# Performance work log

Measured on AMD Instinct MI355X. Metric: run time of the kernel, lower is better.

Reference implementation:

```python
import jax, jax.numpy as jnp
import numpy as np

N_NODES = 50000
N_EDGES = 800000
IN_C = 16
HID_C = 16
OUT_C = 10
N_GRAPHS = 500
EDGE_DIM = 3
MLP_HID = 25
BN_EPS = 1e-5


def setup_inputs() -> dict:
    key = jax.random.key(0)
    ks = iter(jax.random.split(key, 40))

    def nrm(shape, scale=1.0):
        return jax.random.normal(next(ks), shape, dtype=jnp.float32) * scale

    inp = {}
    inp["x"] = nrm((N_NODES, IN_C))
    inp["edge_index"] = jax.random.randint(next(ks), (2, N_EDGES), 0, N_NODES, dtype=jnp.int32)
    inp["edge_attr"] = jax.random.uniform(next(ks), (N_EDGES, EDGE_DIM), dtype=jnp.float32)
    inp["batch"] = jnp.sort(jax.random.randint(next(ks), (N_NODES,), 0, N_GRAPHS, dtype=jnp.int32))

    def bn_params():
        g = jax.random.uniform(next(ks), (MLP_HID,), minval=0.8, maxval=1.2, dtype=jnp.float32)
        b = nrm((MLP_HID,), 0.1)
        mu = nrm((MLP_HID,), 0.1)
        var = jax.random.uniform(next(ks), (MLP_HID,), minval=0.5, maxval=1.5, dtype=jnp.float32)
        return g, b, mu, var

    # edge MLP 1: 3 -> 25 -> IN_C*HID_C
    inp["W1a"] = nrm((EDGE_DIM, MLP_HID), 0.3)
    inp["b1a"] = nrm((MLP_HID,), 0.05)
    inp["g1"], inp["bt1"], inp["m1"], inp["v1"] = bn_params()
    inp["W1b"] = nrm((MLP_HID, IN_C * HID_C), 0.1)
    inp["b1b"] = nrm((IN_C * HID_C,), 0.05)
    inp["root1"] = nrm((IN_C, HID_C), 0.2)
    inp["bias1"] = nrm((HID_C,), 0.05)

    # edge MLP 2: 3 -> 25 -> HID_C*HID_C
    inp["W2a"] = nrm((EDGE_DIM, MLP_HID), 0.3)
    inp["b2a"] = nrm((MLP_HID,), 0.05)
    inp["g2"], inp["bt2"], inp["m2"], inp["v2"] = bn_params()
    inp["W2b"] = nrm((MLP_HID, HID_C * HID_C), 0.1)
    inp["b2b"] = nrm((HID_C * HID_C,), 0.05)
    inp["root2"] = nrm((HID_C, HID_C), 0.2)
    inp["bias2"] = nrm((HID_C,), 0.05)

    # final MLP([HID_C, OUT_C]) -> single plain linear (plain_last)
    inp["fcW"] = nrm((HID_C, OUT_C), 0.2)
    inp["fcb"] = nrm((OUT_C,), 0.05)
    return inp


def _edge_mlp(e, Wa, ba, g, bt, mu, var, Wb, bb):
    # Linear -> BatchNorm(eval) -> ReLU -> (dropout=eval identity) -> Linear
    h = e @ Wa + ba
    h = g * (h - mu) * jax.lax.rsqrt(var + BN_EPS) + bt
    h = jax.nn.relu(h)
    return h @ Wb + bb


def _nnconv(x, src, dst, w_edge, root, bias, out_dim):
    # message: x_j [E,in] times per-edge weight [E,in,out]
    msg = jnp.einsum("ei,eio->eo", x[src], w_edge)
    agg = jax.ops.segment_sum(msg, dst, num_segments=N_NODES)
    deg = jax.ops.segment_sum(jnp.ones((src.shape[0],), msg.dtype), dst, num_segments=N_NODES)
    agg = agg / jnp.maximum(deg, 1.0)[:, None]  # mean aggregation
    return agg + x @ root + bias


def reference(x, edge_index, edge_attr, batch,
              W1a, b1a, g1, bt1, m1, v1, W1b, b1b, root1, bias1,
              W2a, b2a, g2, bt2, m2, v2, W2b, b2b, root2, bias2,
              fcW, fcb):
    src, dst = edge_index[0], edge_index[1]

    w1 = _edge_mlp(edge_attr, W1a, b1a, g1, bt1, m1, v1, W1b, b1b).reshape(-1, IN_C, HID_C)
    x = jax.nn.elu(_nnconv(x, src, dst, w1, root1, bias1, HID_C))

    w2 = _edge_mlp(edge_attr, W2a, b2a, g2, bt2, m2, v2, W2b, b2b).reshape(-1, HID_C, HID_C)
    x = jax.nn.elu(_nnconv(x, src, dst, w2, root2, bias2, HID_C))

    # global mean pooling over graphs
    pooled = jax.ops.segment_sum(x, batch, num_segments=N_GRAPHS)
    cnt = jax.ops.segment_sum(jnp.ones((x.shape[0],), x.dtype), batch, num_segments=N_GRAPHS)
    pooled = pooled / jnp.maximum(cnt, 1.0)[:, None]

    return pooled @ fcW + fcb  # [N_GRAPHS, OUT_C]
```

## Files before the change

### kernel.cpp

```cpp
#include <hip/hip_runtime.h>
#include <math.h>

#define N_NODES 50000
#define N_EDGES 800000
#define IN_C 16
#define HID_C 16
#define OUT_C 10
#define N_GRAPHS 500
#define EDGE_DIM 3
#define MLP_HID 25
#define BN_EPS 1e-5f

#define SCAN_NB ((N_NODES + 255) / 256)
#define NZB 200

typedef __attribute__((ext_vector_type(8))) _Float16 half8;
typedef __attribute__((ext_vector_type(2))) _Float16 half2v;
typedef __attribute__((ext_vector_type(4))) float f32x4;
union U4H8 { uint4 u; half8 h; half2v p[4]; };
union HU { _Float16 h; unsigned short u; };


__global__ __launch_bounds__(256) void setup_kernel(
    const float* __restrict__ W1a, const float* __restrict__ b1a,
    const float* __restrict__ g1, const float* __restrict__ bt1,
    const float* __restrict__ m1, const float* __restrict__ v1,
    const float* __restrict__ W2a, const float* __restrict__ b2a,
    const float* __restrict__ g2, const float* __restrict__ bt2,
    const float* __restrict__ m2, const float* __restrict__ v2,
    const float* __restrict__ W1b, const float* __restrict__ b1b,
    const float* __restrict__ W2b, const float* __restrict__ b2b,
    const int* __restrict__ batch,
    const float* __restrict__ xin, const float* __restrict__ eattr,
    float* __restrict__ AC1, float* __restrict__ AC2,
    unsigned int* __restrict__ WF1, unsigned int* __restrict__ WF2,
    int* __restrict__ goff, int* __restrict__ cnt,
    float4* __restrict__ ea4, unsigned int* __restrict__ xh0,
    int* __restrict__ ticket)
{
    const int blk = blockIdx.x;
    const int tid = threadIdx.x;
    if (blk < 7) {
        int t = blk * 256 + tid;
        if (t >= 1664) return;
        const float *Wb, *bb; unsigned int *WH;
        int tl = t;
        if (t < 832) { Wb = W1b; bb = b1b; WH = WF1; }
        else { tl = t - 832; Wb = W2b; bb = b2b; WH = WF2; }
        int m = tl >> 6;
        int L = tl & 63;
        int q = L >> 4, o = L & 15;
        unsigned int hi[8];
        for (int j = 0; j < 8; ++j) {
            int kp = m*32 + q*8 + j;
            int k = kp >> 4, i = kp & 15;
            float w = (k < 25) ? Wb[k*256 + i*16 + o] : bb[i*16 + o];
            HU cv; cv.h = (_Float16)w;
            hi[j] = cv.u;
        }
        int base = (m*64 + L) * 4;
        for (int d = 0; d < 4; ++d)
            WH[base + d] = hi[2*d] | (hi[2*d+1] << 16);
        return;
    }
    if (blk == 7 || blk == 8) {
        if (blk == 7) {
            if (tid < 26) {
                int k = tid;
                if (k < 25) {
                    float sc = g1[k] / sqrtf(v1[k] + BN_EPS);
                    AC1[k*4+0] = sc * W1a[0*MLP_HID+k];
                    AC1[k*4+1] = sc * W1a[1*MLP_HID+k];
                    AC1[k*4+2] = sc * W1a[2*MLP_HID+k];
                    AC1[k*4+3] = sc * (b1a[k] - m1[k]) + bt1[k];
                } else {
                    AC1[100] = 0.f; AC1[101] = 0.f; AC1[102] = 0.f; AC1[103] = 1.f;
                }
            } else if (tid >= 32 && tid < 58) {
                int k = tid - 32;
                if (k < 25) {
                    float sc = g2[k] / sqrtf(v2[k] + BN_EPS);
                    AC2[k*4+0] = sc * W2a[0*MLP_HID+k];
                    AC2[k*4+1] = sc * W2a[1*MLP_HID+k];
                    AC2[k*4+2] = sc * W2a[2*MLP_HID+k];
                    AC2[k*4+3] = sc * (b2a[k] - m2[k]) + bt2[k];
                } else {
                    AC2[100] = 0.f; AC2[101] = 0.f; AC2[102] = 0.f; AC2[103] = 1.f;
                }
            }
        }
        int g = (blk - 7) * 256 + tid;
        if (g <= N_GRAPHS) {
            int lo = 0, hi = N_NODES;
            while (lo < hi) {
                int mid = (lo + hi) >> 1;
                if (batch[mid] < g) lo = mid + 1; else hi = mid;
            }
            goff[g] = lo;
        }
        return;
    }
    const int bt = (blk - 9) * 256 + tid;
    const int STR = NZB * 256;
    int4* c4 = (int4*)cnt;
    const int4 z4 = {0, 0, 0, 0};
    for (int i = bt; i < 12500; i += STR) c4[i] = z4;
    for (int e = bt; e < N_EDGES; e += STR) {
        float4 a;
        a.x = eattr[e*3+0];
        a.y = eattr[e*3+1];
        a.z = eattr[e*3+2];
        a.w = 0.f;
        ea4[e] = a;
    }
    const float2* x2 = (const float2*)xin;
    for (int i = bt; i < 400000; i += STR) {
        float2 v = x2[i];
        HU h0; h0.h = (_Float16)v.x;
        HU h1; h1.h = (_Float16)v.y;
        xh0[i] = (unsigned int)h0.u | ((unsigned int)h1.u << 16);
    }
    if (blk == 9 && tid == 0) *ticket = 0;
}


__global__ __launch_bounds__(256) void rank_kernel(const int* __restrict__ dst,
                                                   int* __restrict__ cnt,
                                                   int* __restrict__ rank) {
    int e = blockIdx.x * blockDim.x + threadIdx.x;
    if (e < N_EDGES) rank[e] = atomicAdd(&cnt[dst[e]], 1);
}

__global__ __launch_bounds__(256) void scan_p1(const int* __restrict__ cnt,
                                               int* __restrict__ bsum,
                                               int* __restrict__ bpre,
                                               int* __restrict__ off,
                                               int* __restrict__ ticket) {
    __shared__ int lds[256];
    __shared__ int sDone;
    int t = threadIdx.x;
    int idx = blockIdx.x * 256 + t;
    lds[t] = (idx < N_NODES) ? cnt[idx] : 0;
    __syncthreads();
    for (int d = 128; d > 0; d >>= 1) {
        if (t < d) lds[t] += lds[t + d];
        __syncthreads();
    }
    if (t == 0) {
        bsum[blockIdx.x] = lds[0];
        __threadfence();
        sDone = atomicAdd(ticket, 1);
    }
    __syncthreads();
    if (sDone != SCAN_NB - 1) return;
    __threadfence();
    int v = (t < SCAN_NB) ? bsum[t] : 0;
    __syncthreads();
    lds[t] = v;
    __syncthreads();
    for (int d = 1; d < 256; d <<= 1) {
        int u = (t >= d) ? lds[t - d] : 0;
        __syncthreads();
        lds[t] += u;
        __syncthreads();
    }
    if (t < SCAN_NB) bpre[t] = (t > 0) ? lds[t - 1] : 0;
    if (t == 255) off[N_NODES] = lds[255];
}

__global__ __launch_bounds__(256) void scan_p3(const int* __restrict__ cnt,
                                               const int* __restrict__ bpre,
                                               int* __restrict__ off) {
    __shared__ int lds[256];
    int t = threadIdx.x;
    int idx = blockIdx.x * 256 + t;
    int v = (idx < N_NODES) ? cnt[idx] : 0;
    lds[t] = v;
    __syncthreads();
    for (int d = 1; d < 256; d <<= 1) {
        int u = (t >= d) ? lds[t - d] : 0;
        __syncthreads();
        lds[t] += u;
        __syncthreads();
    }
    if (idx < N_NODES) off[idx] = bpre[blockIdx.x] + lds[t] - v;
}


__global__ __launch_bounds__(256) void edge_mfma7_kernel(
    const unsigned short* __restrict__ xh,
    const int* __restrict__ src,
    const int* __restrict__ dst,
    const int* __restrict__ rank,
    const int* __restrict__ off,
    const float4* __restrict__ ea4,
    const float* __restrict__ AC,
    const unsigned int* __restrict__ WF,
    float* __restrict__ msg_buf)
{
    __shared__ uint4 wf_s[832];
    const int tid = threadIdx.x;
    #pragma unroll
    for (int it = 0; it < 4; ++it) {
        int gi = tid + it*256;
        if (gi < 832) wf_s[gi] = ((const uint4*)WF)[gi];
    }
    __syncthreads();

    const int wave = tid >> 6;
    const int lane = tid & 63;
    const int q    = lane >> 4;
    const int el   = lane & 15;
    const int i0   = (q & 1) * 8;
    const bool bsel = (q >> 1) != 0;
    const int E0   = (blockIdx.x * 4 + wave) * 64;

    const int sAll = src[E0 + lane];
    const int dAll = dst[E0 + lane];
    const int rAll = rank[E0 + lane];
    const int pAll = off[dAll] + rAll;

    int   sT[4];
    float a0[4], a1[4], a2[4];
    #pragma unroll
    for (int t = 0; t < 4; ++t) {
        sT[t] = __shfl(sAll, t*16 + el);
        float4 at = ea4[E0 + t*16 + el];
        a0[t] = at.x; a1[t] = at.y; a2[t] = at.z;
    }

    U4H8 xf[4];
    #pragma unroll
    for (int t = 0; t < 4; ++t)
        xf[t].u = *(const uint4*)(const void*)(xh + (size_t)sT[t]*16 + i0);

    f32x4 acc0 = {0.f,0.f,0.f,0.f}, acc1 = {0.f,0.f,0.f,0.f};
    f32x4 acc2 = {0.f,0.f,0.f,0.f}, acc3 = {0.f,0.f,0.f,0.f};
    #pragma unroll 1
    for (int m = 0; m < 13; ++m) {
        const float4 Ae = *(const float4*)(AC + m*8);
        const float4 Ao = *(const float4*)(AC + m*8 + 4);
        const float A0 = bsel ? Ao.x : Ae.x;
        const float A1 = bsel ? Ao.y : Ae.y;
        const float A2 = bsel ? Ao.z : Ae.z;
        const float A3 = bsel ? Ao.w : Ae.w;
        U4H8 w; w.u = wf_s[m*64 + lane];
        #pragma unroll
        for (int t = 0; t < 4; ++t) {
            float h = fmaxf(fmaf(a2[t], A2, fmaf(a1[t], A1,
                              fmaf(a0[t], A0, A3))), 0.f);
            _Float16 hh = (_Float16)h;
            half2v h2; h2.x = hh; h2.y = hh;
            U4H8 f;
            #pragma unroll
            for (int j = 0; j < 4; ++j) f.p[j] = h2 * xf[t].p[j];
            f32x4 a = (t==0) ? acc0 : (t==1) ? acc1 : (t==2) ? acc2 : acc3;
            a = __builtin_amdgcn_mfma_f32_16x16x32_f16(w.h, f.h, a, 0, 0, 0);
            if (t==0) acc0 = a; else if (t==1) acc1 = a;
            else if (t==2) acc2 = a; else acc3 = a;
        }
    }

    #pragma unroll
    for (int t = 0; t < 4; ++t) {
        int row = __shfl(pAll, t*16 + el);
        f32x4 a = (t==0) ? acc0 : (t==1) ? acc1 : (t==2) ? acc2 : acc3;
        *(f32x4*)(msg_buf + (size_t)row * HID_C + q*4) = a;
    }
}

__global__ __launch_bounds__(256) void node_gather_kernel(
    const float* __restrict__ xin, const float* __restrict__ msg_buf,
    const int* __restrict__ off,
    const float* __restrict__ root, const float* __restrict__ bias,
    float* __restrict__ xout, unsigned int* __restrict__ xh_out)
{
    __shared__ float root_s[IN_C * HID_C];
    if (threadIdx.x < 64)
        ((float4*)root_s)[threadIdx.x] = ((const float4*)root)[threadIdx.x];
    __syncthreads();

    int t = blockIdx.x * blockDim.x + threadIdx.x;
    int n = t >> 2;
    if (n >= N_NODES) return;
    int c0 = (t & 3) * 4;
    int lo = off[n], hi = off[n+1];
    float inv = 1.f / fmaxf((float)(hi - lo), 1.f);

    const f32x4* m4 = (const f32x4*)msg_buf;
    const int qi = c0 >> 2;
    f32x4 s0 = {0.f,0.f,0.f,0.f}, s1 = {0.f,0.f,0.f,0.f};
    int r = lo;
    for (; r + 2 <= hi; r += 2) {
        s0 += m4[(size_t)r*4 + qi];
        s1 += m4[(size_t)(r+1)*4 + qi];
    }
    if (r < hi) s0 += m4[(size_t)r*4 + qi];
    f32x4 s = s0 + s1;

    const float4 bv = *(const float4*)(bias + c0);
    f32x4 acc;
    acc.x = fmaf(s.x, inv, bv.x);
    acc.y = fmaf(s.y, inv, bv.y);
    acc.z = fmaf(s.z, inv, bv.z);
    acc.w = fmaf(s.w, inv, bv.w);

    const float4* x4 = (const float4*)(xin + (size_t)n * IN_C);
    #pragma unroll
    for (int j = 0; j < 4; ++j) {
        float4 xv = x4[j];
        #pragma unroll
        for (int k = 0; k < 4; ++k) {
            float xi = (k==0) ? xv.x : (k==1) ? xv.y : (k==2) ? xv.z : xv.w;
            const float4 rv = *(const float4*)(root_s + (j*4+k)*HID_C + c0);
            acc.x = fmaf(xi, rv.x, acc.x);
            acc.y = fmaf(xi, rv.y, acc.y);
            acc.z = fmaf(xi, rv.z, acc.z);
            acc.w = fmaf(xi, rv.w, acc.w);
        }
    }

    acc.x = acc.x > 0.f ? acc.x : (expf(acc.x) - 1.f);
    acc.y = acc.y > 0.f ? acc.y : (expf(acc.y) - 1.f);
    acc.z = acc.z > 0.f ? acc.z : (expf(acc.z) - 1.f);
    acc.w = acc.w > 0.f ? acc.w : (expf(acc.w) - 1.f);
    *(f32x4*)(xout + (size_t)n * HID_C + c0) = acc;

    if (xh_out) {
        HU h0, h1, h2, h3;
        h0.h = (_Float16)acc.x; h1.h = (_Float16)acc.y;
        h2.h = (_Float16)acc.z; h3.h = (_Float16)acc.w;
        uint2 pk;
        pk.x = (unsigned int)h0.u | ((unsigned int)h1.u << 16);
        pk.y = (unsigned int)h2.u | ((unsigned int)h3.u << 16);
        ((uint2*)xh_out)[n*4 + qi] = pk;
    }
}

__global__ __launch_bounds__(64) void pool_final_kernel(
    const float* __restrict__ xin, const int* __restrict__ goff,
    const float* __restrict__ fcW, const float* __restrict__ fcb,
    float* __restrict__ out)
{
    __shared__ float part[4][HID_C];
    __shared__ float pooled[HID_C];
    int g = blockIdx.x;
    int t = threadIdx.x;
    int c = t & 15, sub = t >> 4;
    int lo = goff[g], hi = goff[g+1];
    float s = 0.f;
    for (int n = lo + sub; n < hi; n += 4)
        s += xin[(size_t)n*HID_C + c];
    part[sub][c] = s;
    __syncthreads();
    if (t < HID_C) {
        pooled[t] = (part[0][t] + part[1][t] + part[2][t] + part[3][t])
                    / fmaxf((float)(hi - lo), 1.f);
    }
    __syncthreads();
    if (t < OUT_C) {
        float acc = fcb[t];
        #pragma unroll
        for (int i = 0; i < HID_C; ++i)
            acc = fmaf(pooled[i], fcW[i*OUT_C+t], acc);
        out[g*OUT_C + t] = acc;
    }
}


extern "C" void kernel_launch(void* const* d_in, const int* in_sizes, int n_in,
                              void* d_out, int out_size, void* d_ws, size_t ws_size,
                              hipStream_t stream)
{
    const float* x     = (const float*)d_in[0];
    const int*   ei    = (const int*)d_in[1];
    const float* eattr = (const float*)d_in[2];
    const int*   batch = (const int*)d_in[3];
    const float* W1a   = (const float*)d_in[4];
    const float* b1a   = (const float*)d_in[5];
    const float* g1    = (const float*)d_in[6];
    const float* bt1   = (const float*)d_in[7];
    const float* m1    = (const float*)d_in[8];
    const float* v1    = (const float*)d_in[9];
    const float* W1b   = (const float*)d_in[10];
    const float* b1b   = (const float*)d_in[11];
    const float* root1 = (const float*)d_in[12];
    const float* bias1 = (const float*)d_in[13];
    const float* W2a   = (const float*)d_in[14];
    const float* b2a   = (const float*)d_in[15];
    const float* g2    = (const float*)d_in[16];
    const float* bt2   = (const float*)d_in[17];
    const float* m2    = (const float*)d_in[18];
    const float* v2    = (const float*)d_in[19];
    const float* W2b   = (const float*)d_in[20];
    const float* b2b   = (const float*)d_in[21];
    const float* root2 = (const float*)d_in[22];
    const float* bias2 = (const float*)d_in[23];
    const float* fcW   = (const float*)d_in[24];
    const float* fcb   = (const float*)d_in[25];

    const int* src = ei;
    const int* dst = ei + N_EDGES;

    float* ws   = (float*)d_ws;
    float* MSG  = ws;
    float* X1   = ws + 12800000;
    float* X2   = ws + 13600000;
    int*   RANK = (int*)(ws + 14400000);
    int*   CNT  = (int*)(ws + 15200000);
    int*   OFF  = (int*)(ws + 15250000);
    int*   GOFF = (int*)(ws + 15300064);
    unsigned int* WF1 = (unsigned int*)(ws + 15300576);
    unsigned int* WF2 = (unsigned int*)(ws + 15303904);
    float* AC1  = ws + 15307232;
    float* AC2  = ws + 15307344;
    int*   BSUM = (int*)(ws + 15307456);
    int*   BPRE = (int*)(ws + 15307712);
    int*   TICK = (int*)(ws + 15307968);
    float* EA4  = ws + 15308032;
    unsigned int* XH0 = (unsigned int*)(ws + 18508032);
    unsigned int* XH1 = (unsigned int*)(ws + 18908032);

    setup_kernel<<<9 + NZB, 256, 0, stream>>>(
        W1a, b1a, g1, bt1, m1, v1, W2a, b2a, g2, bt2, m2, v2,
        W1b, b1b, W2b, b2b, batch, x, eattr,
        AC1, AC2, WF1, WF2, GOFF, CNT, (float4*)EA4, XH0, TICK);
    rank_kernel<<<N_EDGES/256, 256, 0, stream>>>(dst, CNT, RANK);
    scan_p1<<<SCAN_NB, 256, 0, stream>>>(CNT, BSUM, BPRE, OFF, TICK);
    scan_p3<<<SCAN_NB, 256, 0, stream>>>(CNT, BPRE, OFF);

    edge_mfma7_kernel<<<N_EDGES/256, 256, 0, stream>>>(
        (const unsigned short*)XH0, src, dst, RANK, OFF,
        (const float4*)EA4, AC1, WF1, MSG);
    node_gather_kernel<<<(N_NODES*4 + 255)/256, 256, 0, stream>>>(
        x, MSG, OFF, root1, bias1, X1, XH1);

    edge_mfma7_kernel<<<N_EDGES/256, 256, 0, stream>>>(
        (const unsigned short*)XH1, src, dst, RANK, OFF,
        (const float4*)EA4, AC2, WF2, MSG);
    node_gather_kernel<<<(N_NODES*4 + 255)/256, 256, 0, stream>>>(
        X1, MSG, OFF, root2, bias2, X2, (unsigned int*)nullptr);

    pool_final_kernel<<<N_GRAPHS, 64, 0, stream>>>(X2, GOFF, fcW, fcb, (float*)d_out);
}
```

Measured before the change: 251.4 us.

## Pre-permute edges into CSR order once and store messages in fp16

Adds a permute kernel that scatters src indices and padded edge attributes into destination-sorted order once. Both edge MFMA passes then read contiguously and write messages at their own position instead of scattering through off/rank lookups. Messages are stored as fp16 rather than fp32, halving message write and read traffic in the node gather. The cost is an extra kernel with a scattered write, plus reduced precision in the per-edge messages before mean aggregation.

```diff
diff --git a/kernel.cpp b/kernel.cpp
--- a/kernel.cpp
+++ b/kernel.cpp
@@ -19,6 +19,15 @@
 typedef __attribute__((ext_vector_type(4))) float f32x4;
 union U4H8 { uint4 u; half8 h; half2v p[4]; };
 union HU { _Float16 h; unsigned short u; };
+union UH2 { unsigned int u; half2v h; };
+
+static __device__ inline f32x4 unpack_h4(uint2 v) {
+    UH2 a, b; a.u = v.x; b.u = v.y;
+    f32x4 r;
+    r.x = (float)a.h.x; r.y = (float)a.h.y;
+    r.z = (float)b.h.x; r.w = (float)b.h.y;
+    return r;
+}
 
 
 __global__ __launch_bounds__(256) void setup_kernel(
@@ -30,13 +39,11 @@
     const float* __restrict__ m2, const float* __restrict__ v2,
     const float* __restrict__ W1b, const float* __restrict__ b1b,
     const float* __restrict__ W2b, const float* __restrict__ b2b,
-    const int* __restrict__ batch,
-    const float* __restrict__ xin, const float* __restrict__ eattr,
+    const int* __restrict__ batch, const float* __restrict__ xin,
     float* __restrict__ AC1, float* __restrict__ AC2,
     unsigned int* __restrict__ WF1, unsigned int* __restrict__ WF2,
     int* __restrict__ goff, int* __restrict__ cnt,
-    float4* __restrict__ ea4, unsigned int* __restrict__ xh0,
-    int* __restrict__ ticket)
+    unsigned int* __restrict__ xh0, int* __restrict__ ticket)
 {
     const int blk = blockIdx.x;
     const int tid = threadIdx.x;
@@ -105,14 +112,6 @@
     int4* c4 = (int4*)cnt;
     const int4 z4 = {0, 0, 0, 0};
     for (int i = bt; i < 12500; i += STR) c4[i] = z4;
-    for (int e = bt; e < N_EDGES; e += STR) {
-        float4 a;
-        a.x = eattr[e*3+0];
-        a.y = eattr[e*3+1];
-        a.z = eattr[e*3+2];
-        a.w = 0.f;
-        ea4[e] = a;
-    }
     const float2* x2 = (const float2*)xin;
     for (int i = bt; i < 400000; i += STR) {
         float2 v = x2[i];
@@ -186,17 +185,32 @@
     if (idx < N_NODES) off[idx] = bpre[blockIdx.x] + lds[t] - v;
 }
 
-
-__global__ __launch_bounds__(256) void edge_mfma7_kernel(
+__global__ __launch_bounds__(256) void permute_kernel(
+    const int* __restrict__ src, const int* __restrict__ dst,
+    const int* __restrict__ rank, const int* __restrict__ off,
+    const float* __restrict__ eattr,
+    int* __restrict__ ssrc, float4* __restrict__ ea4p)
+{
+    int e = blockIdx.x * blockDim.x + threadIdx.x;
+    int d = dst[e];
+    int p = off[d] + rank[e];
+    ssrc[p] = src[e];
+    float4 a;
+    a.x = eattr[e*3+0];
+    a.y = eattr[e*3+1];
+    a.z = eattr[e*3+2];
+    a.w = 0.f;
+    ea4p[p] = a;
+}
+
+
+__global__ __launch_bounds__(256) void edge_mfma8_kernel(
     const unsigned short* __restrict__ xh,
-    const int* __restrict__ src,
-    const int* __restrict__ dst,
-    const int* __restrict__ rank,
-    const int* __restrict__ off,
-    const float4* __restrict__ ea4,
+    const int* __restrict__ ssrc,
+    const float4* __restrict__ ea4p,
     const float* __restrict__ AC,
     const unsigned int* __restrict__ WF,
-    float* __restrict__ msg_buf)
+    unsigned int* __restrict__ msg16)
 {
     __shared__ uint4 wf_s[832];
     const int tid = threadIdx.x;
@@ -213,19 +227,16 @@
     const int el   = lane & 15;
     const int i0   = (q & 1) * 8;
     const bool bsel = (q >> 1) != 0;
-    const int E0   = (blockIdx.x * 4 + wave) * 64;
-
-    const int sAll = src[E0 + lane];
-    const int dAll = dst[E0 + lane];
-    const int rAll = rank[E0 + lane];
-    const int pAll = off[dAll] + rAll;
+    const int P0   = (blockIdx.x * 4 + wave) * 64;
+
+    const int sAll = ssrc[P0 + lane];
 
     int   sT[4];
     float a0[4], a1[4], a2[4];
     #pragma unroll
     for (int t = 0; t < 4; ++t) {
         sT[t] = __shfl(sAll, t*16 + el);
-        float4 at = ea4[E0 + t*16 + el];
+        float4 at = ea4p[P0 + t*16 + el];
         a0[t] = at.x; a1[t] = at.y; a2[t] = at.z;
     }
 
@@ -263,14 +274,19 @@
 
     #pragma unroll
     for (int t = 0; t < 4; ++t) {
-        int row = __shfl(pAll, t*16 + el);
         f32x4 a = (t==0) ? acc0 : (t==1) ? acc1 : (t==2) ? acc2 : acc3;
-        *(f32x4*)(msg_buf + (size_t)row * HID_C + q*4) = a;
+        HU c0, c1, c2, c3;
+        c0.h = (_Float16)a.x; c1.h = (_Float16)a.y;
+        c2.h = (_Float16)a.z; c3.h = (_Float16)a.w;
+        uint2 pk;
+        pk.x = (unsigned int)c0.u | ((unsigned int)c1.u << 16);
+        pk.y = (unsigned int)c2.u | ((unsigned int)c3.u << 16);
+        ((uint2*)msg16)[(size_t)(P0 + t*16 + el) * 4 + q] = pk;
     }
 }
 
 __global__ __launch_bounds__(256) void node_gather_kernel(
-    const float* __restrict__ xin, const float* __restrict__ msg_buf,
+    const float* __restrict__ xin, const unsigned int* __restrict__ msg16,
     const int* __restrict__ off,
     const float* __restrict__ root, const float* __restrict__ bias,
     float* __restrict__ xout, unsigned int* __restrict__ xh_out)
@@ -287,15 +303,15 @@
     int lo = off[n], hi = off[n+1];
     float inv = 1.f / fmaxf((float)(hi - lo), 1.f);
 
-    const f32x4* m4 = (const f32x4*)msg_buf;
+    const uint2* m2 = (const uint2*)msg16;
     const int qi = c0 >> 2;
     f32x4 s0 = {0.f,0.f,0.f,0.f}, s1 = {0.f,0.f,0.f,0.f};
     int r = lo;
     for (; r + 2 <= hi; r += 2) {
-        s0 += m4[(size_t)r*4 + qi];
-        s1 += m4[(size_t)(r+1)*4 + qi];
-    }
-    if (r < hi) s0 += m4[(size_t)r*4 + qi];
+        s0 += unpack_h4(m2[(size_t)r*4 + qi]);
+        s1 += unpack_h4(m2[(size_t)(r+1)*4 + qi]);
+    }
+    if (r < hi) s0 += unpack_h4(m2[(size_t)r*4 + qi]);
     f32x4 s = s0 + s1;
 
     const float4 bv = *(const float4*)(bias + c0);
@@ -403,43 +419,44 @@
     const int* dst = ei + N_EDGES;
 
     float* ws   = (float*)d_ws;
-    float* MSG  = ws;
-    float* X1   = ws + 12800000;
-    float* X2   = ws + 13600000;
-    int*   RANK = (int*)(ws + 14400000);
-    int*   CNT  = (int*)(ws + 15200000);
-    int*   OFF  = (int*)(ws + 15250000);
-    int*   GOFF = (int*)(ws + 15300064);
-    unsigned int* WF1 = (unsigned int*)(ws + 15300576);
-    unsigned int* WF2 = (unsigned int*)(ws + 15303904);
-    float* AC1  = ws + 15307232;
-    float* AC2  = ws + 15307344;
-    int*   BSUM = (int*)(ws + 15307456);
-    int*   BPRE = (int*)(ws + 15307712);
-    int*   TICK = (int*)(ws + 15307968);
-    float* EA4  = ws + 15308032;
-    unsigned int* XH0 = (unsigned int*)(ws + 18508032);
-    unsigned int* XH1 = (unsigned int*)(ws + 18908032);
+    unsigned int* MSG16 = (unsigned int*)ws;
+    float* X1   = ws + 6400000;
+    float* X2   = ws + 7200000;
+    int*   RANK = (int*)(ws + 8000000);
+    int*   CNT  = (int*)(ws + 8800000);
+    int*   OFF  = (int*)(ws + 8850000);
+    int*   GOFF = (int*)(ws + 8900064);
+    unsigned int* WF1 = (unsigned int*)(ws + 8900576);
+    unsigned int* WF2 = (unsigned int*)(ws + 8903904);
+    float* AC1  = ws + 8907232;
+    float* AC2  = ws + 8907344;
+    int*   BSUM = (int*)(ws + 8907456);
+    int*   BPRE = (int*)(ws + 8907712);
+    int*   TICK = (int*)(ws + 8907968);
+    int*   SSRC = (int*)(ws + 8908032);
+    float* EA4P = ws + 9708032;
+    unsigned int* XH0 = (unsigned int*)(ws + 12908032);
+    unsigned int* XH1 = (unsigned int*)(ws + 13308032);
 
     setup_kernel<<<9 + NZB, 256, 0, stream>>>(
         W1a, b1a, g1, bt1, m1, v1, W2a, b2a, g2, bt2, m2, v2,
-        W1b, b1b, W2b, b2b, batch, x, eattr,
-        AC1, AC2, WF1, WF2, GOFF, CNT, (float4*)EA4, XH0, TICK);
+        W1b, b1b, W2b, b2b, batch, x,
+        AC1, AC2, WF1, WF2, GOFF, CNT, XH0, TICK);
     rank_kernel<<<N_EDGES/256, 256, 0, stream>>>(dst, CNT, RANK);
     scan_p1<<<SCAN_NB, 256, 0, stream>>>(CNT, BSUM, BPRE, OFF, TICK);
     scan_p3<<<SCAN_NB, 256, 0, stream>>>(CNT, BPRE, OFF);
-
-    edge_mfma7_kernel<<<N_EDGES/256, 256, 0, stream>>>(
-        (const unsigned short*)XH0, src, dst, RANK, OFF,
-        (const float4*)EA4, AC1, WF1, MSG);
+    permute_kernel<<<N_EDGES/256, 256, 0, stream>>>(src, dst, RANK, OFF, eattr,
+                                                    SSRC, (float4*)EA4P);
+
+    edge_mfma8_kernel<<<N_EDGES/256, 256, 0, stream>>>(
+        (const unsigned short*)XH0, SSRC, (const float4*)EA4P, AC1, WF1, MSG16);
     node_gather_kernel<<<(N_NODES*4 + 255)/256, 256, 0, stream>>>(
-        x, MSG, OFF, root1, bias1, X1, XH1);
-
-    edge_mfma7_kernel<<<N_EDGES/256, 256, 0, stream>>>(
-        (const unsigned short*)XH1, src, dst, RANK, OFF,
-        (const float4*)EA4, AC2, WF2, MSG);
+        x, MSG16, OFF, root1, bias1, X1, XH1);
+
+    edge_mfma8_kernel<<<N_EDGES/256, 256, 0, stream>>>(
+        (const unsigned short*)XH1, SSRC, (const float4*)EA4P, AC2, WF2, MSG16);
     node_gather_kernel<<<(N_NODES*4 + 255)/256, 256, 0, stream>>>(
-        X1, MSG, OFF, root2, bias2, X2, (unsigned int*)nullptr);
+        X1, MSG16, OFF, root2, bias2, X2, (unsigned int*)nullptr);
 
     pool_final_kernel<<<N_GRAPHS, 64, 0, stream>>>(X2, GOFF, fcW, fcb, (float*)d_out);
 }
```

Result: slower. 263.6 us (+4.8%).

## Fuse all stages into one persistent kernel with grid-wide barriers

Applied to the files above, without the earlier changes.

Replaces the nine separate kernel launches (setup, rank, two scan passes, two edge/node pairs, pooling) with one persistent kernel of 256 blocks of 1024 threads. Stages are separated by a software grid barrier built on atomic counters. The scan is rewritten as wave-level shuffle scans over int4 chunks, and pooling runs one graph per wave. This removes launch gaps and tail effects between kernels. In exchange it adds spin-wait barrier cost, assumes all 256 blocks are co-resident, and gives the edge and node phases fewer threads per block with grid-stride loops.

```diff
diff --git a/kernel.cpp b/kernel.cpp
--- a/kernel.cpp
+++ b/kernel.cpp
@@ -11,8 +11,11 @@
 #define MLP_HID 25
 #define BN_EPS 1e-5f
 
-#define SCAN_NB ((N_NODES + 255) / 256)
-#define NZB 200
+#define GRID 256
+#define BLKT 1024
+#define GSZ (GRID * BLKT)
+#define NWAVES (GRID * (BLKT / 64))
+#define NCHUNK 196
 
 typedef __attribute__((ext_vector_type(8))) _Float16 half8;
 typedef __attribute__((ext_vector_type(2))) _Float16 half2v;
@@ -20,29 +23,203 @@
 union U4H8 { uint4 u; half8 h; half2v p[4]; };
 union HU { _Float16 h; unsigned short u; };
 
-
-__global__ __launch_bounds__(256) void setup_kernel(
+__device__ __forceinline__ void gbar(int* bar, int* gen) {
+    __syncthreads();
+    if (threadIdx.x == 0) {
+        __threadfence();
+        int g = __hip_atomic_load(gen, __ATOMIC_RELAXED, __HIP_MEMORY_SCOPE_AGENT);
+        int a = __hip_atomic_fetch_add(bar, 1, __ATOMIC_ACQ_REL, __HIP_MEMORY_SCOPE_AGENT);
+        if (a == GRID - 1) {
+            __hip_atomic_store(bar, 0, __ATOMIC_RELAXED, __HIP_MEMORY_SCOPE_AGENT);
+            __hip_atomic_fetch_add(gen, 1, __ATOMIC_RELEASE, __HIP_MEMORY_SCOPE_AGENT);
+        } else {
+            while (__hip_atomic_load(gen, __ATOMIC_ACQUIRE, __HIP_MEMORY_SCOPE_AGENT) == g) {
+                __builtin_amdgcn_s_sleep(1);
+            }
+        }
+        __threadfence();
+    }
+    __syncthreads();
+}
+
+__device__ __forceinline__ void edge_phase(
+    const unsigned short* __restrict__ xh,
+    const int* __restrict__ src, const int* __restrict__ dst,
+    const int* __restrict__ rank, const int* __restrict__ off,
+    const float4* __restrict__ ea4, const float* __restrict__ AC,
+    const unsigned int* __restrict__ WF, float* __restrict__ msg_buf,
+    uint4* wf_s, int tid)
+{
+    for (int gi = tid; gi < 832; gi += BLKT)
+        wf_s[gi] = ((const uint4*)WF)[gi];
+    __syncthreads();
+
+    const int wave = tid >> 6;
+    const int lane = tid & 63;
+    const int q    = lane >> 4;
+    const int el   = lane & 15;
+    const int i0   = (q & 1) * 8;
+    const bool bsel = (q >> 1) != 0;
+    const int gw   = blockIdx.x * (BLKT / 64) + wave;
+
+    for (int v = gw; v < N_EDGES / 64; v += NWAVES) {
+        const int E0 = v * 64;
+        const int sAll = src[E0 + lane];
+        const int dAll = dst[E0 + lane];
+        const int rAll = rank[E0 + lane];
+        const int pAll = off[dAll] + rAll;
+
+        int   sT[4];
+        float a0[4], a1[4], a2[4];
+        #pragma unroll
+        for (int t = 0; t < 4; ++t) {
+            sT[t] = __shfl(sAll, t*16 + el);
+            float4 at = ea4[E0 + t*16 + el];
+            a0[t] = at.x; a1[t] = at.y; a2[t] = at.z;
+        }
+
+        U4H8 xf[4];
+        #pragma unroll
+        for (int t = 0; t < 4; ++t)
+            xf[t].u = *(const uint4*)(const void*)(xh + (size_t)sT[t]*16 + i0);
+
+        f32x4 acc0 = {0.f,0.f,0.f,0.f}, acc1 = {0.f,0.f,0.f,0.f};
+        f32x4 acc2 = {0.f,0.f,0.f,0.f}, acc3 = {0.f,0.f,0.f,0.f};
+        #pragma unroll 1
+        for (int m = 0; m < 13; ++m) {
+            const float4 Ae = *(const float4*)(AC + m*8);
+            const float4 Ao = *(const float4*)(AC + m*8 + 4);
+            const float A0 = bsel ? Ao.x : Ae.x;
+            const float A1 = bsel ? Ao.y : Ae.y;
+            const float A2 = bsel ? Ao.z : Ae.z;
+            const float A3 = bsel ? Ao.w : Ae.w;
+            U4H8 w; w.u = wf_s[m*64 + lane];
+            #pragma unroll
+            for (int t = 0; t < 4; ++t) {
+                float h = fmaxf(fmaf(a2[t], A2, fmaf(a1[t], A1,
+                                  fmaf(a0[t], A0, A3))), 0.f);
+                _Float16 hh = (_Float16)h;
+                half2v h2; h2.x = hh; h2.y = hh;
+                U4H8 f;
+                #pragma unroll
+                for (int j = 0; j < 4; ++j) f.p[j] = h2 * xf[t].p[j];
+                f32x4 a = (t==0) ? acc0 : (t==1) ? acc1 : (t==2) ? acc2 : acc3;
+                a = __builtin_amdgcn_mfma_f32_16x16x32_f16(w.h, f.h, a, 0, 0, 0);
+                if (t==0) acc0 = a; else if (t==1) acc1 = a;
+                else if (t==2) acc2 = a; else acc3 = a;
+            }
+        }
+
+        #pragma unroll
+        for (int t = 0; t < 4; ++t) {
+            int row = __shfl(pAll, t*16 + el);
+            f32x4 a = (t==0) ? acc0 : (t==1) ? acc1 : (t==2) ? acc2 : acc3;
+            *(f32x4*)(msg_buf + (size_t)row * HID_C + q*4) = a;
+        }
+    }
+}
+
+__device__ __forceinline__ void node_phase(
+    const float* __restrict__ xin, const float* __restrict__ msg_buf,
+    const int* __restrict__ off, const float* root_s,
+    const float* __restrict__ bias,
+    float* __restrict__ xout, unsigned int* __restrict__ xh_out, int gt)
+{
+    for (int t = gt; t < N_NODES * 4; t += GSZ) {
+        int n = t >> 2;
+        int c0 = (t & 3) * 4;
+        int lo = off[n], hi = off[n+1];
+        float inv = 1.f / fmaxf((float)(hi - lo), 1.f);
+
+        const f32x4* m4 = (const f32x4*)msg_buf;
+        const int qi = t & 3;
+        f32x4 s0 = {0.f,0.f,0.f,0.f}, s1 = {0.f,0.f,0.f,0.f};
+        int r = lo;
+        for (; r + 2 <= hi; r += 2) {
+            s0 += m4[(size_t)r*4 + qi];
+            s1 += m4[(size_t)(r+1)*4 + qi];
+        }
+        if (r < hi) s0 += m4[(size_t)r*4 + qi];
+        f32x4 s = s0 + s1;
+
+        const float4 bv = *(const float4*)(bias + c0);
+        f32x4 acc;
+        acc.x = fmaf(s.x, inv, bv.x);
+        acc.y = fmaf(s.y, inv, bv.y);
+        acc.z = fmaf(s.z, inv, bv.z);
+        acc.w = fmaf(s.w, inv, bv.w);
+
+        const float4* x4 = (const float4*)(xin + (size_t)n * IN_C);
+        #pragma unroll
+        for (int j = 0; j < 4; ++j) {
+            float4 xv = x4[j];
+            #pragma unroll
+            for (int k = 0; k < 4; ++k) {
+                float xi = (k==0) ? xv.x : (k==1) ? xv.y : (k==2) ? xv.z : xv.w;
+                const float4 rv = *(const float4*)(root_s + (j*4+k)*HID_C + c0);
+                acc.x = fmaf(xi, rv.x, acc.x);
+                acc.y = fmaf(xi, rv.y, acc.y);
+                acc.z = fmaf(xi, rv.z, acc.z);
+                acc.w = fmaf(xi, rv.w, acc.w);
+            }
+        }
+
+        acc.x = acc.x > 0.f ? acc.x : (expf(acc.x) - 1.f);
+        acc.y = acc.y > 0.f ? acc.y : (expf(acc.y) - 1.f);
+        acc.z = acc.z > 0.f ? acc.z : (expf(acc.z) - 1.f);
+        acc.w = acc.w > 0.f ? acc.w : (expf(acc.w) - 1.f);
+        *(f32x4*)(xout + (size_t)n * HID_C + c0) = acc;
+
+        if (xh_out) {
+            HU h0, h1, h2, h3;
+            h0.h = (_Float16)acc.x; h1.h = (_Float16)acc.y;
+            h2.h = (_Float16)acc.z; h3.h = (_Float16)acc.w;
+            uint2 pk;
+            pk.x = (unsigned int)h0.u | ((unsigned int)h1.u << 16);
+            pk.y = (unsigned int)h2.u | ((unsigned int)h3.u << 16);
+            ((uint2*)xh_out)[n*4 + qi] = pk;
+        }
+    }
+}
+
+__global__ __launch_bounds__(BLKT) void mega_kernel(
+    const float* __restrict__ xin, const int* __restrict__ src,
+    const int* __restrict__ dst, const float* __restrict__ eattr,
+    const int* __restrict__ batch,
     const float* __restrict__ W1a, const float* __restrict__ b1a,
     const float* __restrict__ g1, const float* __restrict__ bt1,
     const float* __restrict__ m1, const float* __restrict__ v1,
+    const float* __restrict__ W1b, const float* __restrict__ b1b,
+    const float* __restrict__ root1, const float* __restrict__ bias1,
     const float* __restrict__ W2a, const float* __restrict__ b2a,
     const float* __restrict__ g2, const float* __restrict__ bt2,
     const float* __restrict__ m2, const float* __restrict__ v2,
-    const float* __restrict__ W1b, const float* __restrict__ b1b,
     const float* __restrict__ W2b, const float* __restrict__ b2b,
-    const int* __restrict__ batch,
-    const float* __restrict__ xin, const float* __restrict__ eattr,
-    float* __restrict__ AC1, float* __restrict__ AC2,
-    unsigned int* __restrict__ WF1, unsigned int* __restrict__ WF2,
-    int* __restrict__ goff, int* __restrict__ cnt,
-    float4* __restrict__ ea4, unsigned int* __restrict__ xh0,
-    int* __restrict__ ticket)
+    const float* __restrict__ root2, const float* __restrict__ bias2,
+    const float* __restrict__ fcW, const float* __restrict__ fcb,
+    float* __restrict__ MSG, float* __restrict__ X1, float* __restrict__ X2,
+    int* __restrict__ RANK, int* __restrict__ CNT, int* __restrict__ OFF,
+    int* __restrict__ GOFF, unsigned int* __restrict__ WF1,
+    unsigned int* __restrict__ WF2, float* __restrict__ AC1,
+    float* __restrict__ AC2, int* __restrict__ BSUM, int* __restrict__ BPRE,
+    float4* __restrict__ EA4, unsigned int* __restrict__ XH0,
+    unsigned int* __restrict__ XH1, float* __restrict__ out,
+    int* __restrict__ ctrl)
 {
-    const int blk = blockIdx.x;
-    const int tid = threadIdx.x;
-    if (blk < 7) {
-        int t = blk * 256 + tid;
-        if (t >= 1664) return;
+    __shared__ uint4 wf_s[832];
+    __shared__ float root_s[IN_C * HID_C];
+    __shared__ int   sc[256];
+
+    const int tid  = threadIdx.x;
+    const int gt   = blockIdx.x * BLKT + tid;
+    const int wave = tid >> 6;
+    const int lane = tid & 63;
+    const int gw   = blockIdx.x * (BLKT / 64) + wave;
+    int* bar = ctrl;
+    int* gen = ctrl + 1;
+
+    if (gt < 1664) {
+        int t = gt;
         const float *Wb, *bb; unsigned int *WH;
         int tl = t;
         if (t < 832) { Wb = W1b; bb = b1b; WH = WF1; }
@@ -61,309 +238,154 @@
         int base = (m*64 + L) * 4;
         for (int d = 0; d < 4; ++d)
             WH[base + d] = hi[2*d] | (hi[2*d+1] << 16);
-        return;
-    }
-    if (blk == 7 || blk == 8) {
-        if (blk == 7) {
-            if (tid < 26) {
-                int k = tid;
-                if (k < 25) {
-                    float sc = g1[k] / sqrtf(v1[k] + BN_EPS);
-                    AC1[k*4+0] = sc * W1a[0*MLP_HID+k];
-                    AC1[k*4+1] = sc * W1a[1*MLP_HID+k];
-                    AC1[k*4+2] = sc * W1a[2*MLP_HID+k];
-                    AC1[k*4+3] = sc * (b1a[k] - m1[k]) + bt1[k];
-                } else {
-                    AC1[100] = 0.f; AC1[101] = 0.f; AC1[102] = 0.f; AC1[103] = 1.f;
-                }
-            } else if (tid >= 32 && tid < 58) {
-                int k = tid - 32;
-                if (k < 25) {
-                    float sc = g2[k] / sqrtf(v2[k] + BN_EPS);
-                    AC2[k*4+0] = sc * W2a[0*MLP_HID+k];
-                    AC2[k*4+1] = sc * W2a[1*MLP_HID+k];
-                    AC2[k*4+2] = sc * W2a[2*MLP_HID+k];
-                    AC2[k*4+3] = sc * (b2a[k] - m2[k]) + bt2[k];
-                } else {
-                    AC2[100] = 0.f; AC2[101] = 0.f; AC2[102] = 0.f; AC2[103] = 1.f;
-                }
-            }
-        }
-        int g = (blk - 7) * 256 + tid;
-        if (g <= N_GRAPHS) {
-            int lo = 0, hi = N_NODES;
-            while (lo < hi) {
-                int mid = (lo + hi) >> 1;
-                if (batch[mid] < g) lo = mid + 1; else hi = mid;
-            }
-            goff[g] = lo;
-        }
-        return;
-    }
-    const int bt = (blk - 9) * 256 + tid;
-    const int STR = NZB * 256;
-    int4* c4 = (int4*)cnt;
-    const int4 z4 = {0, 0, 0, 0};
-    for (int i = bt; i < 12500; i += STR) c4[i] = z4;
-    for (int e = bt; e < N_EDGES; e += STR) {
+    }
+    if (gt < 26) {
+        int k = gt;
+        if (k < 25) {
+            float s = g1[k] / sqrtf(v1[k] + BN_EPS);
+            AC1[k*4+0] = s * W1a[0*MLP_HID+k];
+            AC1[k*4+1] = s * W1a[1*MLP_HID+k];
+            AC1[k*4+2] = s * W1a[2*MLP_HID+k];
+            AC1[k*4+3] = s * (b1a[k] - m1[k]) + bt1[k];
+        } else {
+            AC1[100] = 0.f; AC1[101] = 0.f; AC1[102] = 0.f; AC1[103] = 1.f;
+        }
+    } else if (gt >= 32 && gt < 58) {
+        int k = gt - 32;
+        if (k < 25) {
+            float s = g2[k] / sqrtf(v2[k] + BN_EPS);
+            AC2[k*4+0] = s * W2a[0*MLP_HID+k];
+            AC2[k*4+1] = s * W2a[1*MLP_HID+k];
+            AC2[k*4+2] = s * W2a[2*MLP_HID+k];
+            AC2[k*4+3] = s * (b2a[k] - m2[k]) + bt2[k];
+        } else {
+            AC2[100] = 0.f; AC2[101] = 0.f; AC2[102] = 0.f; AC2[103] = 1.f;
+        }
+    }
+    if (gt <= N_GRAPHS) {
+        int g = gt;
+        int lo = 0, hi = N_NODES;
+        while (lo < hi) {
+            int mid = (lo + hi) >> 1;
+            if (batch[mid] < g) lo = mid + 1; else hi = mid;
+        }
+        GOFF[g] = lo;
+    }
+    {
+        int4* c4 = (int4*)CNT;
+        const int4 z4 = {0,0,0,0};
+        if (gt < 12500) c4[gt] = z4;
+    }
+    for (int e = gt; e < N_EDGES; e += GSZ) {
         float4 a;
         a.x = eattr[e*3+0];
         a.y = eattr[e*3+1];
         a.z = eattr[e*3+2];
         a.w = 0.f;
-        ea4[e] = a;
-    }
-    const float2* x2 = (const float2*)xin;
-    for (int i = bt; i < 400000; i += STR) {
-        float2 v = x2[i];
-        HU h0; h0.h = (_Float16)v.x;
-        HU h1; h1.h = (_Float16)v.y;
-        xh0[i] = (unsigned int)h0.u | ((unsigned int)h1.u << 16);
-    }
-    if (blk == 9 && tid == 0) *ticket = 0;
-}
-
-
-__global__ __launch_bounds__(256) void rank_kernel(const int* __restrict__ dst,
-                                                   int* __restrict__ cnt,
-                                                   int* __restrict__ rank) {
-    int e = blockIdx.x * blockDim.x + threadIdx.x;
-    if (e < N_EDGES) rank[e] = atomicAdd(&cnt[dst[e]], 1);
-}
-
-__global__ __launch_bounds__(256) void scan_p1(const int* __restrict__ cnt,
-                                               int* __restrict__ bsum,
-                                               int* __restrict__ bpre,
-                                               int* __restrict__ off,
-                                               int* __restrict__ ticket) {
-    __shared__ int lds[256];
-    __shared__ int sDone;
-    int t = threadIdx.x;
-    int idx = blockIdx.x * 256 + t;
-    lds[t] = (idx < N_NODES) ? cnt[idx] : 0;
+        EA4[e] = a;
+    }
+    {
+        const float2* x2 = (const float2*)xin;
+        for (int i = gt; i < 400000; i += GSZ) {
+            float2 v = x2[i];
+            HU h0; h0.h = (_Float16)v.x;
+            HU h1; h1.h = (_Float16)v.y;
+            XH0[i] = (unsigned int)h0.u | ((unsigned int)h1.u << 16);
+        }
+    }
+    gbar(bar, gen);
+
+    for (int e = gt; e < N_EDGES; e += GSZ)
+        RANK[e] = atomicAdd(&CNT[dst[e]], 1);
+    gbar(bar, gen);
+
+    if (gw < NCHUNK) {
+        int i4 = gw*64 + lane;
+        int s = 0;
+        if (i4 < 12500) {
+            int4 v = ((const int4*)CNT)[i4];
+            s = v.x + v.y + v.z + v.w;
+        }
+        #pragma unroll
+        for (int d = 1; d < 64; d <<= 1) s += __shfl_xor(s, d);
+        if (lane == 0) BSUM[gw] = s;
+    }
+    gbar(bar, gen);
+
+    if (blockIdx.x == 0) {
+        if (tid < 256) sc[tid] = (tid < NCHUNK) ? BSUM[tid] : 0;
+        __syncthreads();
+        for (int d = 1; d < 256; d <<= 1) {
+            int u = 0;
+            if (tid < 256 && tid >= d) u = sc[tid - d];
+            __syncthreads();
+            if (tid < 256) sc[tid] += u;
+            __syncthreads();
+        }
+        if (tid < NCHUNK) BPRE[tid] = (tid > 0) ? sc[tid-1] : 0;
+        if (tid == 255) OFF[N_NODES] = sc[255];
+    }
+    gbar(bar, gen);
+
+    if (gw < NCHUNK) {
+        int c = gw;
+        int i4 = c*64 + lane;
+        int4 v = {0,0,0,0};
+        if (i4 < 12500) v = ((const int4*)CNT)[i4];
+        int p1 = v.x, p2 = p1 + v.y, p3 = p2 + v.z, tot = p3 + v.w;
+        int run = tot;
+        #pragma unroll
+        for (int d = 1; d < 64; d <<= 1) {
+            int u = __shfl_up(run, d);
+            if (lane >= d) run += u;
+        }
+        int excl = run - tot + BPRE[c];
+        int idx = i4 * 4;
+        if (idx < N_NODES)     OFF[idx]   = excl;
+        if (idx+1 < N_NODES)   OFF[idx+1] = excl + p1;
+        if (idx+2 < N_NODES)   OFF[idx+2] = excl + p2;
+        if (idx+3 < N_NODES)   OFF[idx+3] = excl + p3;
+    }
+    gbar(bar, gen);
+
+    edge_phase((const unsigned short*)XH0, src, dst, RANK, OFF,
+               EA4, AC1, WF1, MSG, wf_s, tid);
+    gbar(bar, gen);
+
+    for (int i = tid; i < 64; i += BLKT)
+        ((float4*)root_s)[i] = ((const float4*)root1)[i];
     __syncthreads();
-    for (int d = 128; d > 0; d >>= 1) {
-        if (t < d) lds[t] += lds[t + d];
-        __syncthreads();
-    }
-    if (t == 0) {
-        bsum[blockIdx.x] = lds[0];
-        __threadfence();
-        sDone = atomicAdd(ticket, 1);
-    }
+    node_phase(xin, MSG, OFF, root_s, bias1, X1, XH1, gt);
+    gbar(bar, gen);
+
+    edge_phase((const unsigned short*)XH1, src, dst, RANK, OFF,
+               EA4, AC2, WF2, MSG, wf_s, tid);
+    gbar(bar, gen);
+
+    for (int i = tid; i < 64; i += BLKT)
+        ((float4*)root_s)[i] = ((const float4*)root2)[i];
     __syncthreads();
-    if (sDone != SCAN_NB - 1) return;
-    __threadfence();
-    int v = (t < SCAN_NB) ? bsum[t] : 0;
-    __syncthreads();
-    lds[t] = v;
-    __syncthreads();
-    for (int d = 1; d < 256; d <<= 1) {
-        int u = (t >= d) ? lds[t - d] : 0;
-        __syncthreads();
-        lds[t] += u;
-        __syncthreads();
-    }
-    if (t < SCAN_NB) bpre[t] = (t > 0) ? lds[t - 1] : 0;
-    if (t == 255) off[N_NODES] = lds[255];
-}
-
-__global__ __launch_bounds__(256) void scan_p3(const int* __restrict__ cnt,
-                                               const int* __restrict__ bpre,
-                                               int* __restrict__ off) {
-    __shared__ int lds[256];
-    int t = threadIdx.x;
-    int idx = blockIdx.x * 256 + t;
-    int v = (idx < N_NODES) ? cnt[idx] : 0;
-    lds[t] = v;
-    __syncthreads();
-    for (int d = 1; d < 256; d <<= 1) {
-        int u = (t >= d) ? lds[t - d] : 0;
-        __syncthreads();
-        lds[t] += u;
-        __syncthreads();
-    }
-    if (idx < N_NODES) off[idx] = bpre[blockIdx.x] + lds[t] - v;
-}
-
-
-__global__ __launch_bounds__(256) void edge_mfma7_kernel(
-    const unsigned short* __restrict__ xh,
-    const int* __restrict__ src,
-    const int* __restrict__ dst,
-    const int* __restrict__ rank,
-    const int* __restrict__ off,
-    const float4* __restrict__ ea4,
-    const float* __restrict__ AC,
-    const unsigned int* __restrict__ WF,
-    float* __restrict__ msg_buf)
-{
-    __shared__ uint4 wf_s[832];
-    const int tid = threadIdx.x;
-    #pragma unroll
-    for (int it = 0; it < 4; ++it) {
-        int gi = tid + it*256;
-        if (gi < 832) wf_s[gi] = ((const uint4*)WF)[gi];
-    }
-    __syncthreads();
-
-    const int wave = tid >> 6;
-    const int lane = tid & 63;
-    const int q    = lane >> 4;
-    const int el   = lane & 15;
-    const int i0   = (q & 1) * 8;
-    const bool bsel = (q >> 1) != 0;
-    const int E0   = (blockIdx.x * 4 + wave) * 64;
-
-    const int sAll = src[E0 + lane];
-    const int dAll = dst[E0 + lane];
-    const int rAll = rank[E0 + lane];
-    const int pAll = off[dAll] + rAll;
-
-    int   sT[4];
-    float a0[4], a1[4], a2[4];
-    #pragma unroll
-    for (int t = 0; t < 4; ++t) {
-        sT[t] = __shfl(sAll, t*16 + el);
-        float4 at = ea4[E0 + t*16 + el];
-        a0[t] = at.x; a1[t] = at.y; a2[t] = at.z;
-    }
-
-    U4H8 xf[4];
-    #pragma unroll
-    for (int t = 0; t < 4; ++t)
-        xf[t].u = *(const uint4*)(const void*)(xh + (size_t)sT[t]*16 + i0);
-
-    f32x4 acc0 = {0.f,0.f,0.f,0.f}, acc1 = {0.f,0.f,0.f,0.f};
-    f32x4 acc2 = {0.f,0.f,0.f,0.f}, acc3 = {0.f,0.f,0.f,0.f};
-    #pragma unroll 1
-    for (int m = 0; m < 13; ++m) {
-        const float4 Ae = *(const float4*)(AC + m*8);
-        const float4 Ao = *(const float4*)(AC + m*8 + 4);
-        const float A0 = bsel ? Ao.x : Ae.x;
-        const float A1 = bsel ? Ao.y : Ae.y;
-        const float A2 = bsel ? Ao.z : Ae.z;
-        const float A3 = bsel ? Ao.w : Ae.w;
-        U4H8 w; w.u = wf_s[m*64 + lane];
-        #pragma unroll
-        for (int t = 0; t < 4; ++t) {
-            float h = fmaxf(fmaf(a2[t], A2, fmaf(a1[t], A1,
-                              fmaf(a0[t], A0, A3))), 0.f);
-            _Float16 hh = (_Float16)h;
-            half2v h2; h2.x = hh; h2.y = hh;
-            U4H8 f;
-            #pragma unroll
-            for (int j = 0; j < 4; ++j) f.p[j] = h2 * xf[t].p[j];
-            f32x4 a = (t==0) ? acc0 : (t==1) ? acc1 : (t==2) ? acc2 : acc3;
-            a = __builtin_amdgcn_mfma_f32_16x16x32_f16(w.h, f.h, a, 0, 0, 0);
-            if (t==0) acc0 = a; else if (t==1) acc1 = a;
-            else if (t==2) acc2 = a; else acc3 = a;
-        }
-    }
-
-    #pragma unroll
-    for (int t = 0; t < 4; ++t) {
-        int row = __shfl(pAll, t*16 + el);
-        f32x4 a = (t==0) ? acc0 : (t==1) ? acc1 : (t==2) ? acc2 : acc3;
-        *(f32x4*)(msg_buf + (size_t)row * HID_C + q*4) = a;
-    }
-}
-
-__global__ __launch_bounds__(256) void node_gather_kernel(
-    const float* __restrict__ xin, const float* __restrict__ msg_buf,
-    const int* __restrict__ off,
-    const float* __restrict__ root, const float* __restrict__ bias,
-    float* __restrict__ xout, unsigned int* __restrict__ xh_out)
-{
-    __shared__ float root_s[IN_C * HID_C];
-    if (threadIdx.x < 64)
-        ((float4*)root_s)[threadIdx.x] = ((const float4*)root)[threadIdx.x];
-    __syncthreads();
-
-    int t = blockIdx.x * blockDim.x + threadIdx.x;
-    int n = t >> 2;
-    if (n >= N_NODES) return;
-    int c0 = (t & 3) * 4;
-    int lo = off[n], hi = off[n+1];
-    float inv = 1.f / fmaxf((float)(hi - lo), 1.f);
-
-    const f32x4* m4 = (const f32x4*)msg_buf;
-    const int qi = c0 >> 2;
-    f32x4 s0 = {0.f,0.f,0.f,0.f}, s1 = {0.f,0.f,0.f,0.f};
-    int r = lo;
-    for (; r + 2 <= hi; r += 2) {
-        s0 += m4[(size_t)r*4 + qi];
-        s1 += m4[(size_t)(r+1)*4 + qi];
-    }
-    if (r < hi) s0 += m4[(size_t)r*4 + qi];
-    f32x4 s = s0 + s1;
-
-    const float4 bv = *(const float4*)(bias + c0);
-    f32x4 acc;
-    acc.x = fmaf(s.x, inv, bv.x);
-    acc.y = fmaf(s.y, inv, bv.y);
-    acc.z = fmaf(s.z, inv, bv.z);
-    acc.w = fmaf(s.w, inv, bv.w);
-
-    const float4* x4 = (const float4*)(xin + (size_t)n * IN_C);
-    #pragma unroll
-    for (int j = 0; j < 4; ++j) {
-        float4 xv = x4[j];
-        #pragma unroll
-        for (int k = 0; k < 4; ++k) {
-            float xi = (k==0) ? xv.x : (k==1) ? xv.y : (k==2) ? xv.z : xv.w;
-            const float4 rv = *(const float4*)(root_s + (j*4+k)*HID_C + c0);
-            acc.x = fmaf(xi, rv.x, acc.x);
-            acc.y = fmaf(xi, rv.y, acc.y);
-            acc.z = fmaf(xi, rv.z, acc.z);
-            acc.w = fmaf(xi, rv.w, acc.w);
-        }
-    }
-
-    acc.x = acc.x > 0.f ? acc.x : (expf(acc.x) - 1.f);
-    acc.y = acc.y > 0.f ? acc.y : (expf(acc.y) - 1.f);
-    acc.z = acc.z > 0.f ? acc.z : (expf(acc.z) - 1.f);
-    acc.w = acc.w > 0.f ? acc.w : (expf(acc.w) - 1.f);
-    *(f32x4*)(xout + (size_t)n * HID_C + c0) = acc;
-
-    if (xh_out) {
-        HU h0, h1, h2, h3;
-        h0.h = (_Float16)acc.x; h1.h = (_Float16)acc.y;
-        h2.h = (_Float16)acc.z; h3.h = (_Float16)acc.w;
-        uint2 pk;
-        pk.x = (unsigned int)h0.u | ((unsigned int)h1.u << 16);
-        pk.y = (unsigned int)h2.u | ((unsigned int)h3.u << 16);
-        ((uint2*)xh_out)[n*4 + qi] = pk;
-    }
-}
-
-__global__ __launch_bounds__(64) void pool_final_kernel(
-    const float* __restrict__ xin, const int* __restrict__ goff,
-    const float* __restrict__ fcW, const float* __restrict__ fcb,
-    float* __restrict__ out)
-{
-    __shared__ float part[4][HID_C];
-    __shared__ float pooled[HID_C];
-    int g = blockIdx.x;
-    int t = threadIdx.x;
-    int c = t & 15, sub = t >> 4;
-    int lo = goff[g], hi = goff[g+1];
-    float s = 0.f;
-    for (int n = lo + sub; n < hi; n += 4)
-        s += xin[(size_t)n*HID_C + c];
-    part[sub][c] = s;
-    __syncthreads();
-    if (t < HID_C) {
-        pooled[t] = (part[0][t] + part[1][t] + part[2][t] + part[3][t])
-                    / fmaxf((float)(hi - lo), 1.f);
-    }
-    __syncthreads();
-    if (t < OUT_C) {
-        float acc = fcb[t];
-        #pragma unroll
-        for (int i = 0; i < HID_C; ++i)
-            acc = fmaf(pooled[i], fcW[i*OUT_C+t], acc);
-        out[g*OUT_C + t] = acc;
+    node_phase(X1, MSG, OFF, root_s, bias2, X2, (unsigned int*)nullptr, gt);
+    gbar(bar, gen);
+
+    if (gw < N_GRAPHS) {
+        int g = gw;
+        int c = lane & 15, sub = lane >> 4;
+        int lo = GOFF[g], hi = GOFF[g+1];
+        float s = 0.f;
+        for (int n = lo + sub; n < hi; n += 4)
+            s += X2[(size_t)n*HID_C + c];
+        s += __shfl_xor(s, 16);
+        s += __shfl_xor(s, 32);
+        float pooled = s / fmaxf((float)(hi - lo), 1.f);
+        float acc = 0.f;
+        if (lane < OUT_C) acc = fcb[lane];
+        #pragma unroll
+        for (int i = 0; i < HID_C; ++i) {
+            float pi = __shfl(pooled, i);
+            if (lane < OUT_C) acc = fmaf(pi, fcW[i*OUT_C + lane], acc);
+        }
+        if (lane < OUT_C) out[g*OUT_C + lane] = acc;
     }
 }
 
@@ -416,30 +438,19 @@
     float* AC2  = ws + 15307344;
     int*   BSUM = (int*)(ws + 15307456);
     int*   BPRE = (int*)(ws + 15307712);
-    int*   TICK = (int*)(ws + 15307968);
+    int*   CTRL = (int*)(ws + 15307968);
     float* EA4  = ws + 15308032;
     unsigned int* XH0 = (unsigned int*)(ws + 18508032);
     unsigned int* XH1 = (unsigned int*)(ws + 18908032);
 
-    setup_kernel<<<9 + NZB, 256, 0, stream>>>(
-        W1a, b1a, g1, bt1, m1, v1, W2a, b2a, g2, bt2, m2, v2,
-        W1b, b1b, W2b, b2b, batch, x, eattr,
-        AC1, AC2, WF1, WF2, GOFF, CNT, (float4*)EA4, XH0, TICK);
-    rank_kernel<<<N_EDGES/256, 256, 0, stream>>>(dst, CNT, RANK);
-    scan_p1<<<SCAN_NB, 256, 0, stream>>>(CNT, BSUM, BPRE, OFF, TICK);
-    scan_p3<<<SCAN_NB, 256, 0, stream>>>(CNT, BPRE, OFF);
-
-    edge_mfma7_kernel<<<N_EDGES/256, 256, 0, stream>>>(
-        (const unsigned short*)XH0, src, dst, RANK, OFF,
-        (const float4*)EA4, AC1, WF1, MSG);
-    node_gather_kernel<<<(N_NODES*4 + 255)/256, 256, 0, stream>>>(
-        x, MSG, OFF, root1, bias1, X1, XH1);
-
-    edge_mfma7_kernel<<<N_EDGES/256, 256, 0, stream>>>(
-        (const unsigned short*)XH1, src, dst, RANK, OFF,
-        (const float4*)EA4, AC2, WF2, MSG);
-    node_gather_kernel<<<(N_NODES*4 + 255)/256, 256, 0, stream>>>(
-        X1, MSG, OFF, root2, bias2, X2, (unsigned int*)nullptr);
-
-    pool_final_kernel<<<N_GRAPHS, 64, 0, stream>>>(X2, GOFF, fcW, fcb, (float*)d_out);
+    hipMemsetAsync(CTRL, 0, 2 * sizeof(int), stream);
+
+    mega_kernel<<<GRID, BLKT, 0, stream>>>(
+        x, src, dst, eattr, batch,
+        W1a, b1a, g1, bt1, m1, v1, W1b, b1b, root1, bias1,
+        W2a, b2a, g2, bt2, m2, v2, W2b, b2b, root2, bias2,
+        fcW, fcb,
+        MSG, X1, X2, RANK, CNT, OFF, GOFF, WF1, WF2,
+        AC1, AC2, BSUM, BPRE, (float4*)EA4, XH0, XH1,
+        (float*)d_out, CTRL);
 }
```

Result: slower. 721.4 us (+186.9%).
